# Performance work log

Measured on AMD Instinct MI355X. Metric: run time of the kernel, lower is better.

## Reference

```python
import jax, jax.numpy as jnp
import numpy as np

CHARB_EPS = 1e-3
CHARB_ALPHA = 0.45
EDGE_ALPHA = 10.0
BOUNDARY_SUPPRESS = 0.1
W_SMOOTH = 0.15
W_SEGCONS = 0.1
SEG_EPS = 1e-6


def charbonnier(x):
    return jnp.power(x * x + CHARB_EPS * CHARB_EPS, CHARB_ALPHA)


def depthwise_sobel(img, kern):
    # img: (B,C,H,W); kern: (3,3) -> depthwise conv, padding=1
    C = img.shape[1]
    k = jnp.broadcast_to(kern[None, None], (C, 1, 3, 3)).astype(img.dtype)
    return jax.lax.conv_general_dilated(
        img, k, window_strides=(1, 1), padding=[(1, 1), (1, 1)],
        dimension_numbers=('NCHW', 'OIHW', 'NCHW'), feature_group_count=C)


def maxpool3(x):
    # 3x3 max pool, stride 1, pad 1 over last two dims (any rank)
    nd = x.ndim
    return jax.lax.reduce_window(
        x, -jnp.inf, jax.lax.max,
        (1,) * (nd - 2) + (3, 3), (1,) * nd,
        [(0, 0)] * (nd - 2) + [(1, 1), (1, 1)])


def compute_segment_boundary(masks):
    # masks: (B,S,H,W) -> boundary (B,1,H,W)
    occ = masks.sum(axis=1, keepdims=True)             # (B,1,H,W)
    b = jnp.clip(maxpool3(occ) - (-maxpool3(-occ)), 0.0, 1.0)
    per = jnp.clip(maxpool3(masks) - (-maxpool3(-masks)), 0.0, 1.0)  # (B,S,H,W)
    b = b + per.sum(axis=1, keepdims=True)
    return jnp.clip(b, 0.0, 1.0)


def boundary_smooth_loss(flow, image, segment_masks):
    sobel_x = jnp.array([[1., 0., -1.], [2., 0., -2.], [1., 0., -1.]], dtype=flow.dtype)
    gx = depthwise_sobel(image, sobel_x)
    gy = depthwise_sobel(image, sobel_x.T)
    img_grad_mag = (jnp.abs(gx) + jnp.abs(gy)).mean(axis=1, keepdims=True)  # (B,1,H,W)
    edge_w = jnp.exp(-EDGE_ALPHA * img_grad_mag)
    boundary = compute_segment_boundary(segment_masks)
    boundary_w = 1.0 - boundary * (1.0 - BOUNDARY_SUPPRESS)
    weights = edge_w * boundary_w                       # (B,1,H,W)

    fx = flow[:, :, :, 1:] - flow[:, :, :, :-1]
    fy = flow[:, :, 1:, :] - flow[:, :, :-1, :]
    wx = weights[:, :, :, 1:]
    wy = weights[:, :, 1:, :]
    loss1 = (charbonnier(fx).mean(axis=1, keepdims=True) * wx).mean()
    loss1 = loss1 + (charbonnier(fy).mean(axis=1, keepdims=True) * wy).mean()
    # second order
    fxx = fx[:, :, :, 1:] - fx[:, :, :, :-1]
    fyy = fy[:, :, 1:, :] - fy[:, :, :-1, :]
    loss2 = charbonnier(fxx).mean() + charbonnier(fyy).mean()
    return W_SMOOTH * (loss1 + 0.5 * loss2)


def segment_consistency_loss(flow, segment_masks):
    # flow: (B,2,H,W); masks: (B,S,H,W)
    mask_sum = jnp.maximum(segment_masks.sum(axis=(-2, -1)), SEG_EPS)  # (B,S)
    mean_flow = jnp.einsum('bchw,bshw->bsc', flow, segment_masks) / mask_sum[..., None]
    diff = flow[:, None] - mean_flow[:, :, :, None, None]              # (B,S,2,H,W)
    diff_sq = (diff * diff).sum(axis=2)                                # (B,S,H,W)
    # charbonnier(sqrt(d)) == (d + eps^2)^alpha (grad-safe at 0)
    var_map = jnp.power(diff_sq + CHARB_EPS * CHARB_EPS, CHARB_ALPHA)
    num_s = jnp.einsum('bshw,bshw->s', var_map, segment_masks)         # (S,)
    w_s = mask_sum.sum(axis=0)                                         # (S,)
    loss_s = num_s / jnp.maximum(w_s, SEG_EPS)
    total = (loss_s * w_s).sum()
    tw = w_s.sum()
    loss = jnp.where(tw > SEG_EPS, total / tw, 0.0)
    return W_SEGCONS * loss


def setup_inputs() -> dict:
    key = jax.random.key(0)
    k1, k2, k3 = jax.random.split(key, 3)
    B, S, H, W = 8, 16, 512, 512
    flow = jax.random.normal(k1, (B, 2, H, W), dtype=jnp.float32)
    image = jax.random.uniform(k2, (B, 3, H, W), dtype=jnp.float32)
    segment_masks = jax.random.uniform(k3, (B, S, H, W), dtype=jnp.float32)
    return {'flow': flow, 'image': image, 'segment_masks': segment_masks}


def reference(flow, image, segment_masks):
    return segment_consistency_loss(flow, segment_masks) + boundary_smooth_loss(flow, image, segment_masks)
```

## Files before the change

### kernel.cpp

```cpp
#include <hip/hip_runtime.h>

#define BB 8
#define SS 16
#define HH 512
#define WW 512
#define HWP (HH*WW)

#define TH 16
#define TW 32
#define HR 18
#define HC 34
#define NH (HR*HC)
#define LW 35

#define WS_MSUM 0
#define WS_FSUM 128
#define WS_MEAN 384
#define WS_ACC  640
#define WS_TOTAL 660

__device__ __forceinline__ float clip01(float x){ return fminf(fmaxf(x, 0.0f), 1.0f); }
__device__ __forceinline__ float pow045(float v){ return exp2f(0.45f * log2f(v)); }
__device__ __forceinline__ float cbn(float x){ return pow045(x*x + 1e-6f); }

__global__ __launch_bounds__(256, 2)
void kA(const float* __restrict__ flow, const float* __restrict__ masks,
        float* __restrict__ ws)
{
    const int b = blockIdx.y;
    const int base = blockIdx.x * 2048;
    const float* fU = flow + (size_t)b * 2 * HWP;
    const float* fV = fU + HWP;
    const float* mb = masks + (size_t)b * SS * HWP;

    float am[SS], au[SS], av[SS];
#pragma unroll
    for (int s = 0; s < SS; ++s){ am[s]=0.f; au[s]=0.f; av[s]=0.f; }

    for (int it = 0; it < 2; ++it){
        const int p = base + it*1024 + threadIdx.x*4;
        const float4 u = *reinterpret_cast<const float4*>(fU + p);
        const float4 v = *reinterpret_cast<const float4*>(fV + p);
#pragma unroll
        for (int s = 0; s < SS; ++s){
            const float4 m = *reinterpret_cast<const float4*>(mb + s*HWP + p);
            am[s] += (m.x + m.y) + (m.z + m.w);
            au[s] += m.x*u.x + m.y*u.y + m.z*u.z + m.w*u.w;
            av[s] += m.x*v.x + m.y*v.y + m.z*v.z + m.w*v.w;
        }
    }

#pragma unroll
    for (int s = 0; s < SS; ++s){
#pragma unroll
        for (int o = 32; o > 0; o >>= 1){
            am[s] += __shfl_down(am[s], o, 64);
            au[s] += __shfl_down(au[s], o, 64);
            av[s] += __shfl_down(av[s], o, 64);
        }
    }
    __shared__ float red[4][3*SS];
    const int lane = threadIdx.x & 63, wv = threadIdx.x >> 6;
    if (lane == 0){
#pragma unroll
        for (int s = 0; s < SS; ++s){
            red[wv][s] = am[s]; red[wv][SS+s] = au[s]; red[wv][2*SS+s] = av[s];
        }
    }
    __syncthreads();
    if (threadIdx.x < 3*SS){
        const int i = threadIdx.x;
        float t = red[0][i] + red[1][i] + red[2][i] + red[3][i];
        const int s = i % SS, kind = i / SS;
        if (kind == 0) atomicAdd(ws + WS_MSUM + b*SS + s, t);
        else           atomicAdd(ws + WS_FSUM + (b*SS + s)*2 + (kind-1), t);
    }
}

__global__ void kB(float* __restrict__ ws)
{
    const int i = threadIdx.x;
    const int bs = i >> 1;
    const float ms = fmaxf(ws[WS_MSUM + bs], 1e-6f);
    ws[WS_MEAN + i] = ws[WS_FSUM + i] / ms;
}

__global__ __launch_bounds__(256, 2)
void kC(const float* __restrict__ flow, const float* __restrict__ image,
        const float* __restrict__ masks, float* __restrict__ ws)
{
    const int b  = blockIdx.z;
    const int h0 = blockIdx.y * TH;
    const int w0 = blockIdx.x * TW;
    const int tid = threadIdx.x;

    __shared__ float sImg[3][HR*LW];
    __shared__ float sFlo[2][HR*LW];
    __shared__ float sOcc[HR*LW];
    __shared__ float sMsk[2][HR*LW];
    __shared__ float sMean[2*SS];
    __shared__ float sRed[4][20];

    if (tid < 2*SS) sMean[tid] = ws[WS_MEAN + b*2*SS + tid];

    int hli[3], cgi[3]; bool hval[3]; bool hin[3]; int hgi[3];
#pragma unroll
    for (int k = 0; k < 3; ++k){
        const int idx = tid + k*256;
        hval[k] = (k < 2) || (tid < NH - 512);
        const int r = idx / HC, c = idx % HC;
        const int gh = h0 - 1 + r, gw = w0 - 1 + c;
        hli[k] = r*LW + c;
        hin[k] = ((unsigned)gh < (unsigned)HH) && ((unsigned)gw < (unsigned)WW);
        hgi[k] = gh*WW + gw;
        const int ch_ = min(max(gh, 0), HH-1);
        const int cw_ = min(max(gw, 0), WW-1);
        cgi[k] = ch_*WW + cw_;
    }

    const float* img = image + (size_t)b * 3 * HWP;
    const float* flo = flow  + (size_t)b * 2 * HWP;
    const float* mb  = masks + (size_t)b * SS * HWP;

#pragma unroll
    for (int k = 0; k < 3; ++k){
        if (hval[k]){
            const bool in = hin[k]; const int gi = hgi[k]; const int li = hli[k];
            sImg[0][li] = in ? img[0*HWP + gi] : 0.f;
            sImg[1][li] = in ? img[1*HWP + gi] : 0.f;
            sImg[2][li] = in ? img[2*HWP + gi] : 0.f;
            sFlo[0][li] = in ? flo[0*HWP + gi] : 0.f;
            sFlo[1][li] = in ? flo[1*HWP + gi] : 0.f;
        }
    }

    float occA[3] = {0.f, 0.f, 0.f};
    float pf[3];

#pragma unroll
    for (int k = 0; k < 3; ++k) if (hval[k]) pf[k] = mb[cgi[k]];
#pragma unroll
    for (int k = 0; k < 3; ++k) if (hval[k]){ sMsk[0][hli[k]] = pf[k]; occA[k] += pf[k]; }
#pragma unroll
    for (int k = 0; k < 3; ++k) if (hval[k]) pf[k] = mb[1*HWP + cgi[k]];
    __syncthreads();

    const int pr  = tid >> 4;
    const int pc2 = (tid & 15) << 1;
    const int R = pr + 1;
    const float fu0 = sFlo[0][R*LW + pc2+1], fu1 = sFlo[0][R*LW + pc2+2];
    const float fv0 = sFlo[1][R*LW + pc2+1], fv1 = sFlo[1][R*LW + pc2+2];

    float numv[SS];
    float perS0 = 0.f, perS1 = 0.f;

#pragma unroll
    for (int s = 0; s < SS; ++s){
        const float* bufc = sMsk[s & 1];
        float cmx[4], cmn[4], mC0 = 0.f, mC1 = 0.f;
#pragma unroll
        for (int j = 0; j < 4; ++j){
            const float a = bufc[(pr  )*LW + pc2 + j];
            const float m = bufc[(pr+1)*LW + pc2 + j];
            const float d = bufc[(pr+2)*LW + pc2 + j];
            cmx[j] = fmaxf(fmaxf(a, m), d);
            cmn[j] = fminf(fminf(a, m), d);
            if (j == 1) mC0 = m;
            if (j == 2) mC1 = m;
        }
        const float rng0 = fmaxf(fmaxf(cmx[0],cmx[1]),cmx[2]) - fminf(fminf(cmn[0],cmn[1]),cmn[2]);
        const float rng1 = fmaxf(fmaxf(cmx[1],cmx[2]),cmx[3]) - fminf(fminf(cmn[1],cmn[2]),cmn[3]);
        perS0 += clip01(rng0);
        perS1 += clip01(rng1);

        const float mu = sMean[2*s], mv = sMean[2*s+1];
        const float d0u = fu0-mu, d0v = fv0-mv, d1u = fu1-mu, d1v = fv1-mv;
        const float vm0 = pow045(d0u*d0u + d0v*d0v + 1e-6f);
        const float vm1 = pow045(d1u*d1u + d1v*d1v + 1e-6f);
        numv[s] = vm0*mC0 + vm1*mC1;

        if (s < SS-1){
#pragma unroll
            for (int k = 0; k < 3; ++k) if (hval[k]){ sMsk[(s+1)&1][hli[k]] = pf[k]; occA[k] += pf[k]; }
            if (s < SS-2){
#pragma unroll
                for (int k = 0; k < 3; ++k) if (hval[k]) pf[k] = mb[(s+2)*HWP + cgi[k]];
            }
            __syncthreads();
        }
    }

#pragma unroll
    for (int k = 0; k < 3; ++k) if (hval[k]) sOcc[hli[k]] = occA[k];
    __syncthreads();

    float ox[4], on[4];
#pragma unroll
    for (int j = 0; j < 4; ++j){
        const float a = sOcc[(pr  )*LW + pc2 + j];
        const float m = sOcc[(pr+1)*LW + pc2 + j];
        const float d = sOcc[(pr+2)*LW + pc2 + j];
        ox[j] = fmaxf(fmaxf(a, m), d);
        on[j] = fminf(fminf(a, m), d);
    }
    const float org0 = fmaxf(fmaxf(ox[0],ox[1]),ox[2]) - fminf(fminf(on[0],on[1]),on[2]);
    const float org1 = fmaxf(fmaxf(ox[1],ox[2]),ox[3]) - fminf(fminf(on[1],on[2]),on[3]);
    const float bnd0 = clip01(clip01(org0) + perS0);
    const float bnd1 = clip01(clip01(org1) + perS1);

    float mag0 = 0.f, mag1 = 0.f;
#pragma unroll
    for (int ch = 0; ch < 3; ++ch){
        float top[4], mid[4], bot[4];
#pragma unroll
        for (int j = 0; j < 4; ++j){
            top[j] = sImg[ch][(pr  )*LW + pc2 + j];
            mid[j] = sImg[ch][(pr+1)*LW + pc2 + j];
            bot[j] = sImg[ch][(pr+2)*LW + pc2 + j];
        }
        float colV0 = top[0] + 2.f*mid[0] + bot[0];
        float colV1 = top[1] + 2.f*mid[1] + bot[1];
        float colV2 = top[2] + 2.f*mid[2] + bot[2];
        float colV3 = top[3] + 2.f*mid[3] + bot[3];
        const float gx0 = colV0 - colV2;
        const float gx1 = colV1 - colV3;
        const float gy0 = (top[0] + 2.f*top[1] + top[2]) - (bot[0] + 2.f*bot[1] + bot[2]);
        const float gy1 = (top[1] + 2.f*top[2] + top[3]) - (bot[1] + 2.f*bot[2] + bot[3]);
        mag0 += fabsf(gx0) + fabsf(gy0);
        mag1 += fabsf(gx1) + fabsf(gy1);
    }
    mag0 *= (1.f/3.f); mag1 *= (1.f/3.f);
    const float wgt0 = expf(-10.f * mag0) * (1.f - 0.9f*bnd0);
    const float wgt1 = expf(-10.f * mag1) * (1.f - 0.9f*bnd1);

    const int gh  = h0 + pr;
    const int gw0 = w0 + pc2;
    const int gw1 = gw0 + 1;

    const float lu = sFlo[0][R*LW + pc2],     lv = sFlo[1][R*LW + pc2];
    const float ru = sFlo[0][R*LW + pc2 + 3], rv = sFlo[1][R*LW + pc2 + 3];
    const float uu0 = sFlo[0][(R-1)*LW + pc2+1], uv0 = sFlo[1][(R-1)*LW + pc2+1];
    const float uu1 = sFlo[0][(R-1)*LW + pc2+2], uv1 = sFlo[1][(R-1)*LW + pc2+2];
    const float du0 = sFlo[0][(R+1)*LW + pc2+1], dv0 = sFlo[1][(R+1)*LW + pc2+1];
    const float du1 = sFlo[0][(R+1)*LW + pc2+2], dv1 = sFlo[1][(R+1)*LW + pc2+2];

    float l1x = 0.f, l1y = 0.f, l2x = 0.f, l2y = 0.f;

    if (gw0 >= 1) l1x += 0.5f * (cbn(fu0 - lu) + cbn(fv0 - lv)) * wgt0;
    l1x += 0.5f * (cbn(fu1 - fu0) + cbn(fv1 - fv0)) * wgt1;
    if (gh >= 1){
        l1y += 0.5f * (cbn(fu0 - uu0) + cbn(fv0 - uv0)) * wgt0;
        l1y += 0.5f * (cbn(fu1 - uu1) + cbn(fv1 - uv1)) * wgt1;
    }
    if (gw0 >= 1) l2x += cbn(fu1 - 2.f*fu0 + lu) + cbn(fv1 - 2.f*fv0 + lv);
    if (gw1 <= WW-2) l2x += cbn(ru - 2.f*fu1 + fu0) + cbn(rv - 2.f*fv1 + fv0);
    if (gh >= 1 && gh <= HH-2){
        l2y += cbn(du0 - 2.f*fu0 + uu0) + cbn(dv0 - 2.f*fv0 + uv0);
        l2y += cbn(du1 - 2.f*fu1 + uu1) + cbn(dv1 - 2.f*fv1 + uv1);
    }

    float vals[20];
#pragma unroll
    for (int s = 0; s < SS; ++s) vals[s] = numv[s];
    vals[16] = l1x; vals[17] = l1y; vals[18] = l2x; vals[19] = l2y;

    const int lane = tid & 63, wv = tid >> 6;
#pragma unroll
    for (int i = 0; i < 20; ++i){
        float v = vals[i];
#pragma unroll
        for (int o = 32; o > 0; o >>= 1) v += __shfl_down(v, o, 64);
        if (lane == 0) sRed[wv][i] = v;
    }
    __syncthreads();
    if (tid < 20){
        const float t = sRed[0][tid] + sRed[1][tid] + sRed[2][tid] + sRed[3][tid];
        atomicAdd(ws + WS_ACC + tid, t);
    }
}

__global__ void kF(const float* __restrict__ ws, float* __restrict__ out)
{
    __shared__ float sw[SS];
    const int t = threadIdx.x;
    if (t < SS){
        float w = 0.f;
        for (int b = 0; b < BB; ++b) w += fmaxf(ws[WS_MSUM + b*SS + t], 1e-6f);
        sw[t] = w;
    }
    __syncthreads();
    if (t == 0){
        float total = 0.f, tw = 0.f;
        for (int s = 0; s < SS; ++s){
            const float w = sw[s];
            total += (ws[WS_ACC + s] / fmaxf(w, 1e-6f)) * w;
            tw += w;
        }
        const float seg = (tw > 1e-6f) ? (total / tw) : 0.f;
        const float l1 = ws[WS_ACC+16] / (8.f*512.f*511.f) + ws[WS_ACC+17] / (8.f*511.f*512.f);
        const float l2 = ws[WS_ACC+18] / (8.f*2.f*512.f*510.f) + ws[WS_ACC+19] / (8.f*2.f*510.f*512.f);
        out[0] = 0.1f*seg + 0.15f*(l1 + 0.5f*l2);
    }
}

extern "C" void kernel_launch(void* const* d_in, const int* in_sizes, int n_in,
                              void* d_out, int out_size, void* d_ws, size_t ws_size,
                              hipStream_t stream)
{
    (void)in_sizes; (void)n_in; (void)out_size; (void)ws_size;
    const float* flow  = (const float*)d_in[0];
    const float* image = (const float*)d_in[1];
    const float* masks = (const float*)d_in[2];
    float* ws  = (float*)d_ws;
    float* out = (float*)d_out;

    (void)hipMemsetAsync(d_ws, 0, WS_TOTAL * sizeof(float), stream);

    dim3 gA(128, BB);
    kA<<<gA, 256, 0, stream>>>(flow, masks, ws);
    kB<<<1, 256, 0, stream>>>(ws);
    dim3 gC(WW/TW, HH/TH, BB);
    kC<<<gC, 256, 0, stream>>>(flow, image, masks, ws);
    kF<<<1, 64, 0, stream>>>(ws, out);
}
```

Before: 376.8 us.

## Split kA work per wave by segment, deepen mask prefetch, remap kC grid

kA now assigns each wave four segments over 512 pixels and launches four times as many blocks. This removes the 48-register accumulator arrays and the shared-memory reduction, so occupancy can rise, at the cost of more global atomics. kC's segment-mask prefetch moves from one to two slices ahead to hide more load latency. kC also uses a flattened 1D grid with a swizzled block-to-tile mapping that interleaves batches, presumably to spread blocks across XCDs or improve L2 locality.

```diff
diff --git a/kernel.cpp b/kernel.cpp
--- a/kernel.cpp
+++ b/kernel.cpp
@@ -23,57 +23,50 @@
 __device__ __forceinline__ float pow045(float v){ return exp2f(0.45f * log2f(v)); }
 __device__ __forceinline__ float cbn(float x){ return pow045(x*x + 1e-6f); }
 
-__global__ __launch_bounds__(256, 2)
+__global__ __launch_bounds__(256, 4)
 void kA(const float* __restrict__ flow, const float* __restrict__ masks,
         float* __restrict__ ws)
 {
-    const int b = blockIdx.y;
-    const int base = blockIdx.x * 2048;
+    const int b    = blockIdx.y;
+    const int wv   = threadIdx.x >> 6;
+    const int lane = threadIdx.x & 63;
+    const int s0   = wv * 4;
+
     const float* fU = flow + (size_t)b * 2 * HWP;
     const float* fV = fU + HWP;
-    const float* mb = masks + (size_t)b * SS * HWP;
-
-    float am[SS], au[SS], av[SS];
-#pragma unroll
-    for (int s = 0; s < SS; ++s){ am[s]=0.f; au[s]=0.f; av[s]=0.f; }
-
-    for (int it = 0; it < 2; ++it){
-        const int p = base + it*1024 + threadIdx.x*4;
+    const float* mb = masks + (size_t)b * SS * HWP + (size_t)s0 * HWP;
+
+    float acc[12];
+#pragma unroll
+    for (int i = 0; i < 12; ++i) acc[i] = 0.f;
+
+#pragma unroll
+    for (int step = 0; step < 2; ++step){
+        const int p = blockIdx.x * 512 + step * 256 + lane * 4;
         const float4 u = *reinterpret_cast<const float4*>(fU + p);
         const float4 v = *reinterpret_cast<const float4*>(fV + p);
 #pragma unroll
-        for (int s = 0; s < SS; ++s){
-            const float4 m = *reinterpret_cast<const float4*>(mb + s*HWP + p);
-            am[s] += (m.x + m.y) + (m.z + m.w);
-            au[s] += m.x*u.x + m.y*u.y + m.z*u.z + m.w*u.w;
-            av[s] += m.x*v.x + m.y*v.y + m.z*v.z + m.w*v.w;
-        }
-    }
-
-#pragma unroll
-    for (int s = 0; s < SS; ++s){
-#pragma unroll
-        for (int o = 32; o > 0; o >>= 1){
-            am[s] += __shfl_down(am[s], o, 64);
-            au[s] += __shfl_down(au[s], o, 64);
-            av[s] += __shfl_down(av[s], o, 64);
-        }
-    }
-    __shared__ float red[4][3*SS];
-    const int lane = threadIdx.x & 63, wv = threadIdx.x >> 6;
+        for (int k = 0; k < 4; ++k){
+            const float4 m = *reinterpret_cast<const float4*>(mb + (size_t)k * HWP + p);
+            acc[3*k  ] += (m.x + m.y) + (m.z + m.w);
+            acc[3*k+1] += m.x*u.x + m.y*u.y + m.z*u.z + m.w*u.w;
+            acc[3*k+2] += m.x*v.x + m.y*v.y + m.z*v.z + m.w*v.w;
+        }
+    }
+
+#pragma unroll
+    for (int i = 0; i < 12; ++i){
+#pragma unroll
+        for (int o = 32; o > 0; o >>= 1) acc[i] += __shfl_down(acc[i], o, 64);
+    }
     if (lane == 0){
 #pragma unroll
-        for (int s = 0; s < SS; ++s){
-            red[wv][s] = am[s]; red[wv][SS+s] = au[s]; red[wv][2*SS+s] = av[s];
-        }
-    }
-    __syncthreads();
-    if (threadIdx.x < 3*SS){
-        const int i = threadIdx.x;
-        float t = red[0][i] + red[1][i] + red[2][i] + red[3][i];
-        const int s = i % SS, kind = i / SS;
-        if (kind == 0) atomicAdd(ws + WS_MSUM + b*SS + s, t);
-        else           atomicAdd(ws + WS_FSUM + (b*SS + s)*2 + (kind-1), t);
+        for (int k = 0; k < 4; ++k){
+            const int s = s0 + k;
+            atomicAdd(ws + WS_MSUM + b*SS + s,           acc[3*k  ]);
+            atomicAdd(ws + WS_FSUM + (b*SS + s)*2 + 0,   acc[3*k+1]);
+            atomicAdd(ws + WS_FSUM + (b*SS + s)*2 + 1,   acc[3*k+2]);
+        }
     }
 }
 
@@ -89,9 +82,12 @@
 void kC(const float* __restrict__ flow, const float* __restrict__ image,
         const float* __restrict__ masks, float* __restrict__ ws)
 {
-    const int b  = blockIdx.z;
-    const int h0 = blockIdx.y * TH;
-    const int w0 = blockIdx.x * TW;
+    const int lin = blockIdx.x;
+    const int wg  = (lin & 7) * 512 + (lin >> 3);
+    const int b   = wg >> 9;
+    const int rem = wg & 511;
+    const int h0  = (rem >> 4) * TH;
+    const int w0  = (rem & 15) * TW;
     const int tid = threadIdx.x;
 
     __shared__ float sImg[3][HR*LW];
@@ -135,14 +131,16 @@
     }
 
     float occA[3] = {0.f, 0.f, 0.f};
-    float pf[3];
-
-#pragma unroll
-    for (int k = 0; k < 3; ++k) if (hval[k]) pf[k] = mb[cgi[k]];
-#pragma unroll
-    for (int k = 0; k < 3; ++k) if (hval[k]){ sMsk[0][hli[k]] = pf[k]; occA[k] += pf[k]; }
+    float pf[3], pg[3], t0[3];
+
+#pragma unroll
+    for (int k = 0; k < 3; ++k) if (hval[k]) t0[k] = mb[cgi[k]];
+#pragma unroll
+    for (int k = 0; k < 3; ++k) if (hval[k]){ sMsk[0][hli[k]] = t0[k]; occA[k] += t0[k]; }
 #pragma unroll
     for (int k = 0; k < 3; ++k) if (hval[k]) pf[k] = mb[1*HWP + cgi[k]];
+#pragma unroll
+    for (int k = 0; k < 3; ++k) if (hval[k]) pg[k] = mb[2*HWP + cgi[k]];
     __syncthreads();
 
     const int pr  = tid >> 4;
@@ -182,9 +180,11 @@
         if (s < SS-1){
 #pragma unroll
             for (int k = 0; k < 3; ++k) if (hval[k]){ sMsk[(s+1)&1][hli[k]] = pf[k]; occA[k] += pf[k]; }
-            if (s < SS-2){
-#pragma unroll
-                for (int k = 0; k < 3; ++k) if (hval[k]) pf[k] = mb[(s+2)*HWP + cgi[k]];
+#pragma unroll
+            for (int k = 0; k < 3; ++k) pf[k] = pg[k];
+            if (s < SS-3){
+#pragma unroll
+                for (int k = 0; k < 3; ++k) if (hval[k]) pg[k] = mb[(s+3)*HWP + cgi[k]];
             }
             __syncthreads();
         }
@@ -316,10 +316,9 @@
 
     (void)hipMemsetAsync(d_ws, 0, WS_TOTAL * sizeof(float), stream);
 
-    dim3 gA(128, BB);
+    dim3 gA(512, BB);
     kA<<<gA, 256, 0, stream>>>(flow, masks, ws);
     kB<<<1, 256, 0, stream>>>(ws);
-    dim3 gC(WW/TW, HH/TH, BB);
-    kC<<<gC, 256, 0, stream>>>(flow, image, masks, ws);
+    kC<<<4096, 256, 0, stream>>>(flow, image, masks, ws);
     kF<<<1, 64, 0, stream>>>(ws, out);
 }
```

New measurement: 652.0 us. +73.0%, slower.

## Split segment-mean reduction across segments per block and raise occupancy bounds

Applied to the files above, without the earlier changes.

Kernel kA now gives each block one (chunk, segment, batch) triple, so it accumulates three scalars instead of 48 per-thread arrays. This removes the heavy register pressure of the old layout, where every thread looped over all 16 segments. Flow is now re-read once per segment, relying on cache, and the number of atomics grows. Launch bounds for kA and kC are raised to allow 4 blocks per CU, which may force register spilling in kC.

```diff
diff --git a/kernel.cpp b/kernel.cpp
--- a/kernel.cpp
+++ b/kernel.cpp
@@ -23,57 +23,47 @@
 __device__ __forceinline__ float pow045(float v){ return exp2f(0.45f * log2f(v)); }
 __device__ __forceinline__ float cbn(float x){ return pow045(x*x + 1e-6f); }
 
-__global__ __launch_bounds__(256, 2)
+__global__ __launch_bounds__(256, 4)
 void kA(const float* __restrict__ flow, const float* __restrict__ masks,
         float* __restrict__ ws)
 {
-    const int b = blockIdx.y;
-    const int base = blockIdx.x * 2048;
-    const float* fU = flow + (size_t)b * 2 * HWP;
+    const int c = blockIdx.x;
+    const int s = blockIdx.y;
+    const int b = blockIdx.z;
+
+    const float* m  = masks + ((size_t)(b*SS + s)) * HWP + c * 16384;
+    const float* fU = flow + (size_t)b * 2 * HWP + c * 16384;
     const float* fV = fU + HWP;
-    const float* mb = masks + (size_t)b * SS * HWP;
-
-    float am[SS], au[SS], av[SS];
-#pragma unroll
-    for (int s = 0; s < SS; ++s){ am[s]=0.f; au[s]=0.f; av[s]=0.f; }
-
-    for (int it = 0; it < 2; ++it){
-        const int p = base + it*1024 + threadIdx.x*4;
-        const float4 u = *reinterpret_cast<const float4*>(fU + p);
-        const float4 v = *reinterpret_cast<const float4*>(fV + p);
-#pragma unroll
-        for (int s = 0; s < SS; ++s){
-            const float4 m = *reinterpret_cast<const float4*>(mb + s*HWP + p);
-            am[s] += (m.x + m.y) + (m.z + m.w);
-            au[s] += m.x*u.x + m.y*u.y + m.z*u.z + m.w*u.w;
-            av[s] += m.x*v.x + m.y*v.y + m.z*v.z + m.w*v.w;
-        }
-    }
-
-#pragma unroll
-    for (int s = 0; s < SS; ++s){
-#pragma unroll
-        for (int o = 32; o > 0; o >>= 1){
-            am[s] += __shfl_down(am[s], o, 64);
-            au[s] += __shfl_down(au[s], o, 64);
-            av[s] += __shfl_down(av[s], o, 64);
-        }
-    }
-    __shared__ float red[4][3*SS];
+
+    float a0 = 0.f, a1 = 0.f, a2 = 0.f;
+
+#pragma unroll 4
+    for (int it = 0; it < 16; ++it){
+        const int p = it * 1024 + threadIdx.x * 4;
+        const float4 mm = *reinterpret_cast<const float4*>(m  + p);
+        const float4 u  = *reinterpret_cast<const float4*>(fU + p);
+        const float4 v  = *reinterpret_cast<const float4*>(fV + p);
+        a0 += (mm.x + mm.y) + (mm.z + mm.w);
+        a1 += mm.x*u.x + mm.y*u.y + mm.z*u.z + mm.w*u.w;
+        a2 += mm.x*v.x + mm.y*v.y + mm.z*v.z + mm.w*v.w;
+    }
+
+#pragma unroll
+    for (int o = 32; o > 0; o >>= 1){
+        a0 += __shfl_down(a0, o, 64);
+        a1 += __shfl_down(a1, o, 64);
+        a2 += __shfl_down(a2, o, 64);
+    }
+
+    __shared__ float red[4][3];
     const int lane = threadIdx.x & 63, wv = threadIdx.x >> 6;
-    if (lane == 0){
-#pragma unroll
-        for (int s = 0; s < SS; ++s){
-            red[wv][s] = am[s]; red[wv][SS+s] = au[s]; red[wv][2*SS+s] = av[s];
-        }
-    }
-    __syncthreads();
-    if (threadIdx.x < 3*SS){
+    if (lane == 0){ red[wv][0] = a0; red[wv][1] = a1; red[wv][2] = a2; }
+    __syncthreads();
+    if (threadIdx.x < 3){
         const int i = threadIdx.x;
-        float t = red[0][i] + red[1][i] + red[2][i] + red[3][i];
-        const int s = i % SS, kind = i / SS;
-        if (kind == 0) atomicAdd(ws + WS_MSUM + b*SS + s, t);
-        else           atomicAdd(ws + WS_FSUM + (b*SS + s)*2 + (kind-1), t);
+        const float t = red[0][i] + red[1][i] + red[2][i] + red[3][i];
+        if (i == 0) atomicAdd(ws + WS_MSUM + b*SS + s, t);
+        else        atomicAdd(ws + WS_FSUM + (b*SS + s)*2 + (i-1), t);
     }
 }
 
@@ -85,7 +75,7 @@
     ws[WS_MEAN + i] = ws[WS_FSUM + i] / ms;
 }
 
-__global__ __launch_bounds__(256, 2)
+__global__ __launch_bounds__(256, 4)
 void kC(const float* __restrict__ flow, const float* __restrict__ image,
         const float* __restrict__ masks, float* __restrict__ ws)
 {
@@ -316,7 +306,7 @@
 
     (void)hipMemsetAsync(d_ws, 0, WS_TOTAL * sizeof(float), stream);
 
-    dim3 gA(128, BB);
+    dim3 gA(16, SS, BB);
     kA<<<gA, 256, 0, stream>>>(flow, masks, ws);
     kB<<<1, 256, 0, stream>>>(ws);
     dim3 gC(WW/TW, HH/TH, BB);
```

Result: slower. 517.3 us (+37.3%).
